# Performance work log

Hardware: AMD Instinct MI355X
Metric: run time of the kernel (lower is better)

Reference implementation:

```python
import jax, jax.numpy as jnp
import numpy as np

EPS = 1e-8
LN_EPS = 1e-5
B, T, VDIM, ADIM, DM = 8, 2048, 1024, 768, 256
HID = 1024  # max(64, min(4*256, 2048))
DELTA_LOW, DELTA_HIGH = 2.0, 6.0
WINDOW = 5.0
GATE_MIN, GATE_MAX = 0.05, 0.95


def layer_norm(x):
    mu = jnp.mean(x, axis=-1, keepdims=True)
    var = jnp.var(x, axis=-1, keepdims=True)
    return (x - mu) / jnp.sqrt(var + LN_EPS)


def l2_normalize(x):
    n = jnp.sqrt(jnp.sum(x * x, axis=-1, keepdims=True))
    return x / jnp.maximum(n, EPS)


def setup_inputs() -> dict:
    key = jax.random.key(0)
    ks = jax.random.split(key, 8)
    inp = {
        "video_seq": jax.random.normal(ks[0], (B, T, VDIM), jnp.float32),
        "audio_seq": jax.random.normal(ks[1], (B, T, ADIM), jnp.float32),
        "Wv": jax.random.normal(ks[2], (VDIM, DM), jnp.float32) * (1.0 / np.sqrt(VDIM)),
        "bv": jnp.zeros((DM,), jnp.float32),
        "Wa": jax.random.normal(ks[3], (ADIM, DM), jnp.float32) * (1.0 / np.sqrt(ADIM)),
        "ba": jnp.zeros((DM,), jnp.float32),
        "theta": jnp.float32(0.0),
        "W1": jax.random.normal(ks[4], (3 * DM, HID), jnp.float32) * (1.0 / np.sqrt(3 * DM)),
        "b1": jnp.zeros((HID,), jnp.float32),
        "W2": jax.random.normal(ks[5], (HID, 1), jnp.float32) * (1.0 / np.sqrt(HID)),
        "b2": jnp.zeros((1,), jnp.float32),
    }
    return inp


def reference(video_seq, audio_seq, Wv, bv, Wa, ba, theta, W1, b1, W2, b2):
    v = layer_norm(video_seq @ Wv + bv)          # [B,T,DM]
    a = layer_norm(audio_seq @ Wa + ba)          # [B,T,DM]
    b, t, d = v.shape

    # LearnableDelay
    th = jnp.clip(theta, -12.0, 12.0)
    delta = DELTA_LOW + (DELTA_HIGH - DELTA_LOW) * jax.nn.sigmoid(th)
    delta_b = jnp.full((b,), delta, jnp.float32)

    # SoftTemporalShift (right shift with linear interpolation)
    dl = jnp.clip(delta_b, 0.0, float(t - 1))[:, None, None]   # [B,1,1]
    n = jnp.floor(dl)
    alpha = dl - n
    n_i = n.astype(jnp.int32)
    tidx = jnp.arange(t, dtype=jnp.int32)[None, :, None]       # [1,T,1]
    idx0 = jnp.clip(tidx - n_i, 0, t - 1)                      # [B,T,1]
    idx1 = jnp.clip(idx0 + 1, 0, t - 1)
    a0 = jnp.take_along_axis(a, jnp.broadcast_to(idx0, (b, t, d)), axis=1)
    a1 = jnp.take_along_axis(a, jnp.broadcast_to(idx1, (b, t, d)), axis=1)
    a_shift = (1.0 - alpha) * a0 + alpha * a1

    # DisplacementAwareCausalMask (hard, single scale)
    tf = jnp.arange(t, dtype=jnp.float32)
    tt = tf[None, :, None]                                     # t  -> [1,T,1]
    tau = tf[None, None, :]                                    # tau -> [1,1,T]
    center = jnp.minimum(jnp.maximum(tt + delta_b[:, None, None], 0.0), tt)
    raw = (jnp.abs(tau - center) <= WINDOW).astype(jnp.float32)
    raw = raw * (tau <= tt).astype(jnp.float32)
    M = raw / jnp.maximum(jnp.sum(raw, axis=-1, keepdims=True), EPS)  # [B,T,T]

    # mask-weighted audio context
    a_ctx = jnp.einsum('btk,bkd->btd', M, a_shift)

    # AlignmentGate (dropout inactive at eval)
    vn = l2_normalize(v)
    an = l2_normalize(a_ctx)
    x = jnp.concatenate([an, vn, an * vn], axis=-1)            # [B,T,3*DM]
    h = jax.nn.gelu(x @ W1 + b1, approximate=False)
    logits = jnp.clip(h @ W2 + b2, -12.0, 12.0)                # [B,T,1]
    g = jnp.clip(jax.nn.sigmoid(logits), GATE_MIN, GATE_MAX)

    fused = g * a_ctx + (1.0 - g) * v                          # [B,T,DM]
    return fused
```

## Files before the change

kernel.cpp:

```cpp
#include <hip/hip_runtime.h>
#include <cstdint>
#include <cstddef>

typedef unsigned short u16;
typedef unsigned int u32;
typedef __attribute__((ext_vector_type(8))) short short8;
typedef __attribute__((ext_vector_type(4))) float f32x4;

#define T_SEQ 2048
#define BT_ROWS 16384

__device__ __forceinline__ u16 f2bf(float x) {
  union { float f; u32 u; } v; v.f = x;
  u32 r = v.u + 0x7fffu + ((v.u >> 16) & 1u);
  return (u16)(r >> 16);
}
__device__ __forceinline__ u32 pkbf(float lo, float hi) {
  union { float f; u32 u; } a, b; a.f = lo; b.f = hi;
  const u32 ra = a.u + 0x7fffu + ((a.u >> 16) & 1u);
  const u32 rb = b.u + 0x7fffu + ((b.u >> 16) & 1u);
  return __builtin_amdgcn_perm(rb, ra, 0x07060302);
}
__device__ __forceinline__ float wave_bcast_sum(float x) {
#pragma unroll
  for (int off = 32; off > 0; off >>= 1) x += __shfl_down(x, off);
  return __shfl(x, 0);
}
__device__ __forceinline__ void gl_lds16(const void* g, void* l) {
  __builtin_amdgcn_global_load_lds((const __attribute__((address_space(1))) u32*)g,
                                   (__attribute__((address_space(3))) u32*)l, 16, 0, 0);
}
__device__ __forceinline__ float gelu_f(float x) {
  float z = 1.5957691216057308f * x * (1.0f + 0.044715f * x * x);
  float e = __expf(z);
  return x - x * __builtin_amdgcn_rcpf(1.0f + e);
}

__global__ __launch_bounds__(256) void tcvt_all(const float* __restrict__ Wv,
                                                const float* __restrict__ Wa,
                                                const float* __restrict__ W1,
                                                u16* __restrict__ wvT,
                                                u16* __restrict__ waT,
                                                u16* __restrict__ w1T) {
  __shared__ float tile[32][33];
  int b = blockIdx.x;
  const float* in; u16* out; int K, N, bx, by;
  if (b < 256)      { in = Wv; out = wvT; K = 1024; N = 256;  bx = b & 31;  by = b >> 5; }
  else if (b < 448) { b -= 256; in = Wa; out = waT; K = 768; N = 256;  bx = b % 24; by = b / 24; }
  else              { b -= 448; in = W1; out = w1T; K = 768; N = 1024; bx = b % 24; by = b / 24; }
  const int k0 = bx * 32, n0 = by * 32;
  const int tx = threadIdx.x & 31, ty = threadIdx.x >> 5;
#pragma unroll
  for (int r = 0; r < 4; r++)
    tile[ty + r * 8][tx] = in[(size_t)(k0 + ty + r * 8) * N + n0 + tx];
  __syncthreads();
#pragma unroll
  for (int r = 0; r < 4; r++)
    out[(size_t)(n0 + ty + r * 8) * K + k0 + tx] = f2bf(tile[tx][ty + r * 8]);
}

__global__ __launch_bounds__(256, 5) void gemm_proj(const float* __restrict__ Vin,
                                                    const float* __restrict__ Ain,
                                                    const u16* __restrict__ wvT,
                                                    const u16* __restrict__ waT,
                                                    float* __restrict__ Cv,
                                                    float* __restrict__ Ca) {
  __shared__ float Asf[64 * 64];
  __shared__ u16 Bs[128 * 64];
  int b = blockIdx.x;
  const float* A; const u16* Bt; float* C; int K;
  if (b < 512) { A = Vin; Bt = wvT; C = Cv; K = 1024; }
  else         { b -= 512; A = Ain; Bt = waT; C = Ca; K = 768; }
  const int m0 = (b >> 1) * 64;
  const int n0 = (b & 1) * 128;
  const int tid = threadIdx.x;
  const int wave = tid >> 6, lane = tid & 63, qm = lane & 15, quad = lane >> 4;
  const int rw = (wave >> 1) * 32, cw = (wave & 1) * 64;

  const int arow = tid >> 4;
  const int apart = (tid & 15) ^ (arow & 15);
  const float* Ap[4];
#pragma unroll
  for (int g = 0; g < 4; g++)
    Ap[g] = A + (size_t)(m0 + arow + g * 16) * K + apart * 4;
  const int brow = tid >> 3;
  const int bpart = (tid & 7) ^ (brow & 7);
  const u16* Bp[4];
#pragma unroll
  for (int g = 0; g < 4; g++)
    Bp[g] = Bt + (size_t)(n0 + brow + g * 32) * K + bpart * 8;

  f32x4 acc[2][4] = {};
  for (int kt = 0; kt < K; kt += 64) {
#pragma unroll
    for (int g = 0; g < 4; g++) gl_lds16(Ap[g] + kt, &Asf[(tid + g * 256) * 4]);
#pragma unroll
    for (int g = 0; g < 4; g++) gl_lds16(Bp[g] + kt, &Bs[(tid + g * 256) * 8]);
    __syncthreads();
#pragma unroll
    for (int s = 0; s < 2; s++) {
      short8 af[2], bfr[4];
#pragma unroll
      for (int i = 0; i < 2; i++) {
        const int r = rw + i * 16 + qm;
        const int pb = s * 8 + quad * 2;
        const float4 f0 = *(const float4*)&Asf[r * 64 + ((pb) ^ (r & 15)) * 4];
        const float4 f1 = *(const float4*)&Asf[r * 64 + ((pb + 1) ^ (r & 15)) * 4];
        u32 w[4] = {pkbf(f0.x, f0.y), pkbf(f0.z, f0.w), pkbf(f1.x, f1.y), pkbf(f1.z, f1.w)};
        af[i] = *(short8*)w;
      }
#pragma unroll
      for (int j = 0; j < 4; j++) {
        const int r = cw + j * 16 + qm;
        bfr[j] = *(const short8*)&Bs[r * 64 + ((s * 4 + quad) ^ (r & 7)) * 8];
      }
#pragma unroll
      for (int i = 0; i < 2; i++)
#pragma unroll
        for (int j = 0; j < 4; j++)
          acc[i][j] = __builtin_amdgcn_mfma_f32_16x16x32_bf16(af[i], bfr[j], acc[i][j], 0, 0, 0);
    }
    __syncthreads();
  }
#pragma unroll
  for (int i = 0; i < 2; i++) {
    const int row = m0 + rw + i * 16 + quad * 4;
#pragma unroll
    for (int j = 0; j < 4; j++) {
      const int col = n0 + cw + j * 16 + qm;
#pragma unroll
      for (int r = 0; r < 4; r++)
        C[(size_t)(row + r) * 256 + col] = acc[i][j][r];
    }
  }
}

__global__ __launch_bounds__(256, 6) void gemm_gelu_w2(const u16* __restrict__ Axb,
                                                       const u16* __restrict__ Bt,
                                                       const float* __restrict__ b1,
                                                       const float* __restrict__ W2,
                                                       float* __restrict__ logits) {
  constexpr int K = 768;
  __shared__ u16 As[64 * 64];
  __shared__ u16 Bs[128 * 64];
  const int tid = threadIdx.x;
  const int n0 = blockIdx.x * 128;
  const int m0 = blockIdx.y * 64;
  const int wave = tid >> 6, lane = tid & 63, qm = lane & 15, quad = lane >> 4;
  const int rw = (wave >> 1) * 32, cw = (wave & 1) * 64;

  const int crow = tid >> 3;
  const int cpart = (tid & 7) ^ (crow & 7);
  const u16* Ap[2];
#pragma unroll
  for (int g = 0; g < 2; g++)
    Ap[g] = Axb + (size_t)(m0 + crow + g * 32) * K + cpart * 8;
  const u16* Bp[4];
#pragma unroll
  for (int g = 0; g < 4; g++)
    Bp[g] = Bt + (size_t)(n0 + crow + g * 32) * K + cpart * 8;

  f32x4 acc[2][4] = {};
  for (int kt = 0; kt < K; kt += 64) {
#pragma unroll
    for (int g = 0; g < 2; g++) gl_lds16(Ap[g] + kt, &As[(tid + g * 256) * 8]);
#pragma unroll
    for (int g = 0; g < 4; g++) gl_lds16(Bp[g] + kt, &Bs[(tid + g * 256) * 8]);
    __syncthreads();
#pragma unroll
    for (int s = 0; s < 2; s++) {
      short8 af[2], bfr[4];
#pragma unroll
      for (int i = 0; i < 2; i++) {
        const int r = rw + i * 16 + qm;
        af[i] = *(const short8*)&As[r * 64 + ((s * 4 + quad) ^ (r & 7)) * 8];
      }
#pragma unroll
      for (int j = 0; j < 4; j++) {
        const int r = cw + j * 16 + qm;
        bfr[j] = *(const short8*)&Bs[r * 64 + ((s * 4 + quad) ^ (r & 7)) * 8];
      }
#pragma unroll
      for (int i = 0; i < 2; i++)
#pragma unroll
        for (int j = 0; j < 4; j++)
          acc[i][j] = __builtin_amdgcn_mfma_f32_16x16x32_bf16(af[i], bfr[j], acc[i][j], 0, 0, 0);
    }
    __syncthreads();
  }

  float w2j[4], bc[4];
#pragma unroll
  for (int j = 0; j < 4; j++) {
    const int col = n0 + cw + j * 16 + qm;
    w2j[j] = W2[col];
    bc[j] = b1[col];
  }
#pragma unroll
  for (int i = 0; i < 2; i++) {
#pragma unroll
    for (int r = 0; r < 4; r++) {
      float p = 0.0f;
#pragma unroll
      for (int j = 0; j < 4; j++)
        p += gelu_f(acc[i][j][r] + bc[j]) * w2j[j];
      p += __shfl_xor(p, 1);
      p += __shfl_xor(p, 2);
      p += __shfl_xor(p, 4);
      p += __shfl_xor(p, 8);
      if (qm == 0)
        atomicAdd(&logits[m0 + rw + i * 16 + quad * 4 + r], p);
    }
  }
}

__global__ __launch_bounds__(256) void ln2(float* __restrict__ v, float* __restrict__ a,
                                           const float* __restrict__ bv,
                                           const float* __restrict__ ba) {
  const int gr = blockIdx.x * 4 + (threadIdx.x >> 6);
  const int lane = threadIdx.x & 63;
  float* X; const float* bias; int row;
  if (gr < BT_ROWS) { X = v; bias = bv; row = gr; }
  else              { X = a; bias = ba; row = gr - BT_ROWS; }
  float4 x = *(float4*)&X[(size_t)row * 256 + lane * 4];
  const float4 b = *(const float4*)&bias[lane * 4];
  x.x += b.x; x.y += b.y; x.z += b.z; x.w += b.w;
  float s = x.x + x.y + x.z + x.w;
  float s2 = x.x * x.x + x.y * x.y + x.z * x.z + x.w * x.w;
  s = wave_bcast_sum(s);
  s2 = wave_bcast_sum(s2);
  const float mu = s * (1.0f / 256.0f);
  const float var = s2 * (1.0f / 256.0f) - mu * mu;
  const float inv = rsqrtf(var + 1e-5f);
  x.x = (x.x - mu) * inv; x.y = (x.y - mu) * inv;
  x.z = (x.z - mu) * inv; x.w = (x.w - mu) * inv;
  *(float4*)&X[(size_t)row * 256 + lane * 4] = x;
}

__global__ __launch_bounds__(256) void shift_norm(const float* __restrict__ a,
                                                  const float* __restrict__ v,
                                                  float* __restrict__ actx,
                                                  u16* __restrict__ xb,
                                                  const float* __restrict__ theta) {
  const int row = blockIdx.x * 4 + (threadIdx.x >> 6);
  const int lane = threadIdx.x & 63;
  const int d4 = lane * 4;
  const int bb = row >> 11;
  const int t = row & (T_SEQ - 1);
  const float th = fminf(fmaxf(theta[0], -12.0f), 12.0f);
  const float delta = 2.0f + 4.0f * (1.0f / (1.0f + expf(-th)));
  const float dl = fminf(fmaxf(delta, 0.0f), (float)(T_SEQ - 1));
  const float nf = floorf(dl);
  const float alpha = dl - nf;
  const int ni = (int)nf;
  const float center = fminf(fmaxf((float)t + delta, 0.0f), (float)t);
  float sx = 0, sy = 0, sz = 0, sw = 0, cnt = 0.0f;
  const float* ab = a + (size_t)bb * T_SEQ * 256;
#pragma unroll
  for (int j = 0; j < 6; j++) {
    const int tau = t - 5 + j;
    if (tau < 0) continue;
    if (fabsf((float)tau - center) > 5.0f) continue;
    cnt += 1.0f;
    const int i0 = min(max(tau - ni, 0), T_SEQ - 1);
    const int i1 = min(i0 + 1, T_SEQ - 1);
    const float4 a0 = *(const float4*)&ab[(size_t)i0 * 256 + d4];
    const float4 a1 = *(const float4*)&ab[(size_t)i1 * 256 + d4];
    sx += a0.x + alpha * (a1.x - a0.x);
    sy += a0.y + alpha * (a1.y - a0.y);
    sz += a0.z + alpha * (a1.z - a0.z);
    sw += a0.w + alpha * (a1.w - a0.w);
  }
  const float sc = 1.0f / fmaxf(cnt, 1e-8f);
  float4 o; o.x = sx * sc; o.y = sy * sc; o.z = sz * sc; o.w = sw * sc;
  *(float4*)&actx[(size_t)row * 256 + d4] = o;
  const float4 vv = *(const float4*)&v[(size_t)row * 256 + d4];
  float sa2 = o.x * o.x + o.y * o.y + o.z * o.z + o.w * o.w;
  float sv2 = vv.x * vv.x + vv.y * vv.y + vv.z * vv.z + vv.w * vv.w;
  sa2 = wave_bcast_sum(sa2);
  sv2 = wave_bcast_sum(sv2);
  const float ia = 1.0f / fmaxf(sqrtf(sa2), 1e-8f);
  const float iv = 1.0f / fmaxf(sqrtf(sv2), 1e-8f);
  const float anx = o.x * ia, any_ = o.y * ia, anz = o.z * ia, anw = o.w * ia;
  const float vnx = vv.x * iv, vny = vv.y * iv, vnz = vv.z * iv, vnw = vv.w * iv;
  u16* xr = xb + (size_t)row * 768;
  u32 pa[2] = {pkbf(anx, any_), pkbf(anz, anw)};
  u32 pv[2] = {pkbf(vnx, vny), pkbf(vnz, vnw)};
  u32 pp[2] = {pkbf(anx * vnx, any_ * vny), pkbf(anz * vnz, anw * vnw)};
  *(uint2*)&xr[d4] = *(uint2*)pa;
  *(uint2*)&xr[256 + d4] = *(uint2*)pv;
  *(uint2*)&xr[512 + d4] = *(uint2*)pp;
}

__global__ __launch_bounds__(256) void gate_mix(const float* __restrict__ logits,
                                                const float* __restrict__ b2,
                                                const float* __restrict__ actx,
                                                const float* __restrict__ v,
                                                float* __restrict__ out) {
  const int row = blockIdx.x * 4 + (threadIdx.x >> 6);
  const int lane = threadIdx.x & 63;
  const float l = fminf(fmaxf(logits[row] + b2[0], -12.0f), 12.0f);
  float g = 1.0f / (1.0f + expf(-l));
  g = fminf(fmaxf(g, 0.05f), 0.95f);
  const float4 aa = *(const float4*)&actx[(size_t)row * 256 + lane * 4];
  const float4 vv = *(const float4*)&v[(size_t)row * 256 + lane * 4];
  float4 o;
  o.x = g * aa.x + (1.0f - g) * vv.x;
  o.y = g * aa.y + (1.0f - g) * vv.y;
  o.z = g * aa.z + (1.0f - g) * vv.z;
  o.w = g * aa.w + (1.0f - g) * vv.w;
  *(float4*)&out[(size_t)row * 256 + lane * 4] = o;
}

extern "C" void kernel_launch(void* const* d_in, const int* in_sizes, int n_in,
                              void* d_out, int out_size, void* d_ws, size_t ws_size,
                              hipStream_t stream) {
  const float* video = (const float*)d_in[0];
  const float* audio = (const float*)d_in[1];
  const float* Wv    = (const float*)d_in[2];
  const float* bv    = (const float*)d_in[3];
  const float* Wa    = (const float*)d_in[4];
  const float* ba    = (const float*)d_in[5];
  const float* theta = (const float*)d_in[6];
  const float* W1    = (const float*)d_in[7];
  const float* b1    = (const float*)d_in[8];
  const float* W2    = (const float*)d_in[9];
  const float* b2    = (const float*)d_in[10];
  float* out = (float*)d_out;
  char* ws = (char*)d_ws;

  const size_t OFF_WVT = 0;
  const size_t OFF_WAT = 524288;
  const size_t OFF_W1T = 917504;
  const size_t OFF_LOG = 2490368;
  const size_t OFF_V   = 2555904;
  const size_t OFF_A   = 19333120;
  const size_t OFF_ACTX= 36110336;
  const size_t OFF_XB  = 52887552;

  u16* wvT = (u16*)(ws + OFF_WVT);
  u16* waT = (u16*)(ws + OFF_WAT);
  u16* w1T = (u16*)(ws + OFF_W1T);
  float* logits = (float*)(ws + OFF_LOG);
  float* v    = (float*)(ws + OFF_V);
  float* a    = (float*)(ws + OFF_A);
  float* actx = (float*)(ws + OFF_ACTX);
  u16* xb = (u16*)(ws + OFF_XB);

  tcvt_all<<<1216, 256, 0, stream>>>(Wv, Wa, W1, wvT, waT, w1T);
  hipMemsetAsync(logits, 0, BT_ROWS * sizeof(float), stream);
  gemm_proj<<<1024, 256, 0, stream>>>(video, audio, wvT, waT, v, a);
  ln2<<<2 * BT_ROWS / 4, 256, 0, stream>>>(v, a, bv, ba);
  shift_norm<<<BT_ROWS / 4, 256, 0, stream>>>(a, v, actx, xb, theta);
  gemm_gelu_w2<<<dim3(8, BT_ROWS / 64), 256, 0, stream>>>(xb, w1T, b1, W2, logits);
  gate_mix<<<BT_ROWS / 4, 256, 0, stream>>>(logits, b2, actx, v, out);
}
```

Baseline: 259.3 us.

## Fuse bias and layernorm into projection GEMM epilogue; fold logits memset

The projection GEMM now has each block compute a full 32x256 row tile, so the bias add and layernorm can run in the epilogue through a cross-wave LDS reduction. This removes the separate ln2 pass, which reread and rewrote the v and a buffers. The logits zeroing moves into extra blocks of the weight-transpose kernel, replacing a hipMemsetAsync. In exchange each block reloads the whole weight matrix for fewer rows, and the LDS footprint grows.

```diff
diff --git a/kernel.cpp b/kernel.cpp
--- a/kernel.cpp
+++ b/kernel.cpp
@@ -41,9 +41,14 @@
                                                 const float* __restrict__ W1,
                                                 u16* __restrict__ wvT,
                                                 u16* __restrict__ waT,
-                                                u16* __restrict__ w1T) {
+                                                u16* __restrict__ w1T,
+                                                float* __restrict__ logits) {
+  int b = blockIdx.x;
+  if (b >= 1216) {
+    logits[(b - 1216) * 256 + threadIdx.x] = 0.0f;
+    return;
+  }
   __shared__ float tile[32][33];
-  int b = blockIdx.x;
   const float* in; u16* out; int K, N, bx, by;
   if (b < 256)      { in = Wv; out = wvT; K = 1024; N = 256;  bx = b & 31;  by = b >> 5; }
   else if (b < 448) { b -= 256; in = Wa; out = waT; K = 768; N = 256;  bx = b % 24; by = b / 24; }
@@ -59,50 +64,49 @@
     out[(size_t)(n0 + ty + r * 8) * K + k0 + tx] = f2bf(tile[tx][ty + r * 8]);
 }
 
-__global__ __launch_bounds__(256, 5) void gemm_proj(const float* __restrict__ Vin,
-                                                    const float* __restrict__ Ain,
-                                                    const u16* __restrict__ wvT,
-                                                    const u16* __restrict__ waT,
-                                                    float* __restrict__ Cv,
-                                                    float* __restrict__ Ca) {
-  __shared__ float Asf[64 * 64];
-  __shared__ u16 Bs[128 * 64];
+__global__ __launch_bounds__(256, 4) void proj_ln(const float* __restrict__ Vin,
+                                                  const float* __restrict__ Ain,
+                                                  const u16* __restrict__ wvT,
+                                                  const u16* __restrict__ waT,
+                                                  const float* __restrict__ bv,
+                                                  const float* __restrict__ ba,
+                                                  float* __restrict__ vOut,
+                                                  float* __restrict__ aOut) {
+  __shared__ float Asf[32 * 64];
+  __shared__ u16 Bs[256 * 64];
   int b = blockIdx.x;
-  const float* A; const u16* Bt; float* C; int K;
-  if (b < 512) { A = Vin; Bt = wvT; C = Cv; K = 1024; }
-  else         { b -= 512; A = Ain; Bt = waT; C = Ca; K = 768; }
-  const int m0 = (b >> 1) * 64;
-  const int n0 = (b & 1) * 128;
+  const float* A; const u16* Bt; const float* bias; float* C; int K;
+  if (b < 512) { A = Vin; Bt = wvT; bias = bv; C = vOut; K = 1024; }
+  else         { b -= 512; A = Ain; Bt = waT; bias = ba; C = aOut; K = 768; }
+  const int m0 = b * 32;
   const int tid = threadIdx.x;
   const int wave = tid >> 6, lane = tid & 63, qm = lane & 15, quad = lane >> 4;
-  const int rw = (wave >> 1) * 32, cw = (wave & 1) * 64;
+  const int cw = wave * 64;
 
   const int arow = tid >> 4;
   const int apart = (tid & 15) ^ (arow & 15);
-  const float* Ap[4];
-#pragma unroll
-  for (int g = 0; g < 4; g++)
-    Ap[g] = A + (size_t)(m0 + arow + g * 16) * K + apart * 4;
+  const float* Ap0 = A + (size_t)(m0 + arow) * K + apart * 4;
+  const float* Ap1 = Ap0 + (size_t)16 * K;
   const int brow = tid >> 3;
   const int bpart = (tid & 7) ^ (brow & 7);
-  const u16* Bp[4];
-#pragma unroll
-  for (int g = 0; g < 4; g++)
-    Bp[g] = Bt + (size_t)(n0 + brow + g * 32) * K + bpart * 8;
+  const u16* Bp[8];
+#pragma unroll
+  for (int g = 0; g < 8; g++)
+    Bp[g] = Bt + (size_t)(brow + g * 32) * K + bpart * 8;
 
   f32x4 acc[2][4] = {};
   for (int kt = 0; kt < K; kt += 64) {
-#pragma unroll
-    for (int g = 0; g < 4; g++) gl_lds16(Ap[g] + kt, &Asf[(tid + g * 256) * 4]);
-#pragma unroll
-    for (int g = 0; g < 4; g++) gl_lds16(Bp[g] + kt, &Bs[(tid + g * 256) * 8]);
+    gl_lds16(Ap0 + kt, &Asf[tid * 4]);
+    gl_lds16(Ap1 + kt, &Asf[(tid + 256) * 4]);
+#pragma unroll
+    for (int g = 0; g < 8; g++) gl_lds16(Bp[g] + kt, &Bs[(tid + g * 256) * 8]);
     __syncthreads();
 #pragma unroll
     for (int s = 0; s < 2; s++) {
       short8 af[2], bfr[4];
 #pragma unroll
       for (int i = 0; i < 2; i++) {
-        const int r = rw + i * 16 + qm;
+        const int r = i * 16 + qm;
         const int pb = s * 8 + quad * 2;
         const float4 f0 = *(const float4*)&Asf[r * 64 + ((pb) ^ (r & 15)) * 4];
         const float4 f1 = *(const float4*)&Asf[r * 64 + ((pb + 1) ^ (r & 15)) * 4];
@@ -122,17 +126,60 @@
     }
     __syncthreads();
   }
-#pragma unroll
-  for (int i = 0; i < 2; i++) {
-    const int row = m0 + rw + i * 16 + quad * 4;
-#pragma unroll
-    for (int j = 0; j < 4; j++) {
-      const int col = n0 + cw + j * 16 + qm;
+
+  float bcol[4];
+#pragma unroll
+  for (int j = 0; j < 4; j++) bcol[j] = bias[cw + j * 16 + qm];
+#pragma unroll
+  for (int i = 0; i < 2; i++)
+#pragma unroll
+    for (int j = 0; j < 4; j++)
 #pragma unroll
       for (int r = 0; r < 4; r++)
-        C[(size_t)(row + r) * 256 + col] = acc[i][j][r];
-    }
-  }
+        acc[i][j][r] += bcol[j];
+  float s1[2][4], s2[2][4];
+#pragma unroll
+  for (int i = 0; i < 2; i++)
+#pragma unroll
+    for (int r = 0; r < 4; r++) {
+      float a1 = 0, a2 = 0;
+#pragma unroll
+      for (int j = 0; j < 4; j++) { a1 += acc[i][j][r]; a2 += acc[i][j][r] * acc[i][j][r]; }
+#pragma unroll
+      for (int off = 1; off < 16; off <<= 1) {
+        a1 += __shfl_xor(a1, off);
+        a2 += __shfl_xor(a2, off);
+      }
+      s1[i][r] = a1; s2[i][r] = a2;
+    }
+  float* red = Asf;
+  if (qm == 0) {
+#pragma unroll
+    for (int i = 0; i < 2; i++)
+#pragma unroll
+      for (int r = 0; r < 4; r++) {
+        const int row = i * 16 + quad * 4 + r;
+        red[row * 8 + wave * 2] = s1[i][r];
+        red[row * 8 + wave * 2 + 1] = s2[i][r];
+      }
+  }
+  __syncthreads();
+#pragma unroll
+  for (int i = 0; i < 2; i++)
+#pragma unroll
+    for (int r = 0; r < 4; r++) {
+      const int row = i * 16 + quad * 4 + r;
+      const float4 q1 = *(const float4*)&red[row * 8];
+      const float4 q2 = *(const float4*)&red[row * 8 + 4];
+      const float st = q1.x + q1.z + q2.x + q2.z;
+      const float st2 = q1.y + q1.w + q2.y + q2.w;
+      const float mu = st * (1.0f / 256.0f);
+      const float var = st2 * (1.0f / 256.0f) - mu * mu;
+      const float inv = rsqrtf(var + 1e-5f);
+#pragma unroll
+      for (int j = 0; j < 4; j++)
+        C[(size_t)(m0 + row) * 256 + cw + j * 16 + qm] = (acc[i][j][r] - mu) * inv;
+    }
 }
 
 __global__ __launch_bounds__(256, 6) void gemm_gelu_w2(const u16* __restrict__ Axb,
@@ -212,29 +259,6 @@
         atomicAdd(&logits[m0 + rw + i * 16 + quad * 4 + r], p);
     }
   }
-}
-
-__global__ __launch_bounds__(256) void ln2(float* __restrict__ v, float* __restrict__ a,
-                                           const float* __restrict__ bv,
-                                           const float* __restrict__ ba) {
-  const int gr = blockIdx.x * 4 + (threadIdx.x >> 6);
-  const int lane = threadIdx.x & 63;
-  float* X; const float* bias; int row;
-  if (gr < BT_ROWS) { X = v; bias = bv; row = gr; }
-  else              { X = a; bias = ba; row = gr - BT_ROWS; }
-  float4 x = *(float4*)&X[(size_t)row * 256 + lane * 4];
-  const float4 b = *(const float4*)&bias[lane * 4];
-  x.x += b.x; x.y += b.y; x.z += b.z; x.w += b.w;
-  float s = x.x + x.y + x.z + x.w;
-  float s2 = x.x * x.x + x.y * x.y + x.z * x.z + x.w * x.w;
-  s = wave_bcast_sum(s);
-  s2 = wave_bcast_sum(s2);
-  const float mu = s * (1.0f / 256.0f);
-  const float var = s2 * (1.0f / 256.0f) - mu * mu;
-  const float inv = rsqrtf(var + 1e-5f);
-  x.x = (x.x - mu) * inv; x.y = (x.y - mu) * inv;
-  x.z = (x.z - mu) * inv; x.w = (x.w - mu) * inv;
-  *(float4*)&X[(size_t)row * 256 + lane * 4] = x;
 }
 
 __global__ __launch_bounds__(256) void shift_norm(const float* __restrict__ a,
@@ -347,10 +371,8 @@
   float* actx = (float*)(ws + OFF_ACTX);
   u16* xb = (u16*)(ws + OFF_XB);
 
-  tcvt_all<<<1216, 256, 0, stream>>>(Wv, Wa, W1, wvT, waT, w1T);
-  hipMemsetAsync(logits, 0, BT_ROWS * sizeof(float), stream);
-  gemm_proj<<<1024, 256, 0, stream>>>(video, audio, wvT, waT, v, a);
-  ln2<<<2 * BT_ROWS / 4, 256, 0, stream>>>(v, a, bv, ba);
+  tcvt_all<<<1280, 256, 0, stream>>>(Wv, Wa, W1, wvT, waT, w1T, logits);
+  proj_ln<<<1024, 256, 0, stream>>>(video, audio, wvT, waT, bv, ba, v, a);
   shift_norm<<<BT_ROWS / 4, 256, 0, stream>>>(a, v, actx, xb, theta);
   gemm_gelu_w2<<<dim3(8, BT_ROWS / 64), 256, 0, stream>>>(xb, w1T, b1, W2, logits);
   gate_mix<<<BT_ROWS / 4, 256, 0, stream>>>(logits, b2, actx, v, out);
```

Result: faster. 248.7 us (-4.1%).
